# Kernel tuning notes

Hardware: AMD Instinct MI355X
Metric: run time of the kernel (lower is better)

## Reference

```python
import jax, jax.numpy as jnp
import numpy as np

B, S, T, D, H, DF = 2, 2048, 2048, 1024, 16, 4096
DK = D // H
EPS = 1e-5


def _linear_params(key, d_in, d_out):
    kw, kb = jax.random.split(key)
    s = 1.0 / np.sqrt(d_in)
    W = jax.random.uniform(kw, (d_out, d_in), jnp.float32, -s, s)
    b = jax.random.uniform(kb, (d_out,), jnp.float32, -s, s)
    return W, b


def setup_inputs() -> dict:
    key = jax.random.key(0)
    ks = jax.random.split(key, 16)
    inp = {}
    inp['x'] = jax.random.normal(ks[0], (B, S, D), jnp.float32)
    inp['enc_out'] = jax.random.normal(ks[1], (B, T, D), jnp.float32)
    inp['src_mask'] = jnp.ones((B, 1, 1, T), jnp.int32)
    inp['tgt_mask'] = jnp.tril(jnp.ones((S, S), jnp.int32))[None, None, :, :]
    # self-attn params
    for i, nm in enumerate(['q1', 'k1', 'v1', 'o1']):
        W, b = _linear_params(ks[2 + i], D, D)
        inp['W' + nm], inp['b' + nm] = W, b
    # cross-attn params
    for i, nm in enumerate(['q2', 'k2', 'v2', 'o2']):
        W, b = _linear_params(ks[6 + i], D, D)
        inp['W' + nm], inp['b' + nm] = W, b
    # FFN
    inp['Wf1'], inp['bf1'] = _linear_params(ks[10], D, DF)
    inp['Wf2'], inp['bf2'] = _linear_params(ks[11], DF, D)
    # LayerNorms
    for i in (1, 2, 3):
        inp[f'g{i}'] = jnp.ones((D,), jnp.float32)
        inp[f'be{i}'] = jnp.zeros((D,), jnp.float32)
    return inp


def _lin(x, W, b):
    return x @ W.T + b


def _ln(x, g, b):
    mu = jnp.mean(x, -1, keepdims=True)
    var = jnp.mean(jnp.square(x - mu), -1, keepdims=True)
    return (x - mu) * jax.lax.rsqrt(var + EPS) * g + b


def _mha(q_in, k_in, v_in, Wq, bq, Wk, bk, Wv, bv, Wo, bo, mask):
    Bq = q_in.shape[0]
    q = _lin(q_in, Wq, bq).reshape(Bq, -1, H, DK).transpose(0, 2, 1, 3)
    k = _lin(k_in, Wk, bk).reshape(Bq, -1, H, DK).transpose(0, 2, 1, 3)
    v = _lin(v_in, Wv, bv).reshape(Bq, -1, H, DK).transpose(0, 2, 1, 3)
    scores = jnp.einsum('bhqd,bhkd->bhqk', q, k) / np.sqrt(DK)
    scores = jnp.where(mask == 0, -jnp.inf, scores)
    attn = jax.nn.softmax(scores, axis=-1)
    out = jnp.einsum('bhqk,bhkd->bhqd', attn, v)
    out = out.transpose(0, 2, 1, 3).reshape(Bq, -1, H * DK)
    return _lin(out, Wo, bo)


def reference(x, enc_out, src_mask, tgt_mask,
              Wq1, bq1, Wk1, bk1, Wv1, bv1, Wo1, bo1,
              Wq2, bq2, Wk2, bk2, Wv2, bv2, Wo2, bo2,
              Wf1, bf1, Wf2, bf2,
              g1, be1, g2, be2, g3, be3):
    out = _mha(x, x, x, Wq1, bq1, Wk1, bk1, Wv1, bv1, Wo1, bo1, tgt_mask)
    x = _ln(x + out, g1, be1)
    out = _mha(x, enc_out, enc_out, Wq2, bq2, Wk2, bk2, Wv2, bv2, Wo2, bo2, src_mask)
    x = _ln(x + out, g2, be2)
    ff = _lin(jax.nn.relu(_lin(x, Wf1, bf1)), Wf2, bf2)
    return _ln(x + ff, g3, be3)
```

## Files before the change

kernel.cpp:

```cpp
#include <hip/hip_runtime.h>


typedef __bf16 bf16_t;
typedef bf16_t  bf16x8 __attribute__((ext_vector_type(8)));
typedef float   f32x4  __attribute__((ext_vector_type(4)));
typedef unsigned short ushort_t;
typedef ushort_t u16x8 __attribute__((ext_vector_type(8)));
typedef ushort_t u16x4 __attribute__((ext_vector_type(4)));

__device__ __forceinline__ float b2f(ushort_t u) {
    union { unsigned u; float f; } x; x.u = ((unsigned)u) << 16; return x.f;
}
__device__ __forceinline__ ushort_t f2b(float f) {
    union { float f; unsigned u; } x; x.f = f;
    unsigned r = x.u + 0x7fffu + ((x.u >> 16) & 1u);
    return (ushort_t)(r >> 16);
}
__device__ __forceinline__ unsigned pk2(float lo, float hi) {
    union { float f; unsigned u; } a, b; a.f = lo; b.f = hi;
    return (b.u & 0xffff0000u) | (a.u >> 16);
}

#define GLL(gp, lp)                                                            \
    __builtin_amdgcn_global_load_lds(                                          \
        (const __attribute__((address_space(1))) void*)(gp),                   \
        (__attribute__((address_space(3))) void*)(lp), 16, 0, 0)

__global__ __launch_bounds__(256) void conv_all(
    const float* __restrict__ x,   const float* __restrict__ enc,
    const float* __restrict__ w0, const float* __restrict__ w1,
    const float* __restrict__ w2, const float* __restrict__ w3,
    const float* __restrict__ w4, const float* __restrict__ w5,
    const float* __restrict__ w6, const float* __restrict__ w7,
    const float* __restrict__ wf1, const float* __restrict__ wf2,
    ushort_t* __restrict__ Xb, ushort_t* __restrict__ Eb,
    ushort_t* __restrict__ Wb)
{
    const int b = blockIdx.x;
    const float* src;
    ushort_t* dst;
    size_t blk;
    if (b < 2048)      { src = x;   dst = Xb; blk = b; }
    else if (b < 4096) { src = enc; dst = Eb; blk = b - 2048; }
    else if (b < 8192) {
        const int i = (b - 4096) >> 9;
        src = (i < 4) ? (i < 2 ? (i == 0 ? w0 : w1) : (i == 2 ? w2 : w3))
                      : (i < 6 ? (i == 4 ? w4 : w5) : (i == 6 ? w6 : w7));
        dst = Wb + (size_t)i * 1048576;
        blk = (b - 4096) & 511;
    }
    else if (b < 10240) { src = wf1; dst = Wb + (size_t)8  * 1048576; blk = b - 8192; }
    else                { src = wf2; dst = Wb + (size_t)12 * 1048576; blk = b - 10240; }

    const size_t e = blk * 2048 + (size_t)threadIdx.x * 8;
    const float4 a = *(const float4*)(src + e);
    const float4 c = *(const float4*)(src + e + 4);
    uint4 r;
    r.x = pk2(a.x, a.y); r.y = pk2(a.z, a.w);
    r.z = pk2(c.x, c.y); r.w = pk2(c.z, c.w);
    *(uint4*)(dst + e) = r;
}

template <int EPI, int TM, bool RF32, bool FUSED, bool SPLITA, bool SPLITC>
__global__ __launch_bounds__(256) void gemm_bt(
    const ushort_t* __restrict__ A, const ushort_t* __restrict__ A2,
    const ushort_t* __restrict__ W,
    const float* __restrict__ b1, const float* __restrict__ b2,
    const float* __restrict__ b3,
    const void* __restrict__ Rv,
    ushort_t* __restrict__ C, ushort_t* __restrict__ C2,
    int M, int N, int K)
{
    constexpr int IM = TM / 32;
    __shared__ __align__(16) ushort_t At[TM * 32];
    __shared__ __align__(16) ushort_t Bt[128 * 32];

    const int tid  = threadIdx.x;
    const int lane = tid & 63, w = tid >> 6;
    const int g = lane >> 4, qi = lane & 15;
    const int bm = blockIdx.y * TM, bn = blockIdx.x * 128;
    const int wm = (w >> 1) * (TM / 2), wn = (w & 1) * 64;

    const ushort_t* Ap = SPLITA ? ((bm < 2048) ? A : A2) : A;
    const int       am = SPLITA ? (bm & 2047) : bm;

    const int srow = lane >> 2;
    const int scol = (lane & 3) * 8;

    f32x4 acc[IM][4] = {};

    const int niter = K >> 5;
    for (int kt = 0; kt < niter; ++kt) {
        const int k0 = kt << 5;
        __syncthreads();
        if (TM == 128) {
#pragma unroll
            for (int c = 0; c < 2; ++c) {
                const int s = c * 4 + w;
                GLL(Ap + (size_t)(am + s * 16 + srow) * K + k0 + scol, At + s * 512);
            }
        } else {
            GLL(Ap + (size_t)(am + w * 16 + srow) * K + k0 + scol, At + w * 512);
        }
#pragma unroll
        for (int c = 0; c < 2; ++c) {
            const int s = c * 4 + w;
            GLL(W + (size_t)(bn + s * 16 + srow) * K + k0 + scol, Bt + s * 512);
        }
        __syncthreads();

        bf16x8 af[IM], bfr[4];
#pragma unroll
        for (int i = 0; i < IM; ++i)
            af[i] = *(const bf16x8*)(At + (wm + i * 16 + qi) * 32 + g * 8);
#pragma unroll
        for (int j = 0; j < 4; ++j)
            bfr[j] = *(const bf16x8*)(Bt + (wn + j * 16 + qi) * 32 + g * 8);
#pragma unroll
        for (int i = 0; i < IM; ++i)
#pragma unroll
            for (int j = 0; j < 4; ++j)
                acc[i][j] = __builtin_amdgcn_mfma_f32_16x16x32_bf16(
                    af[i], bfr[j], acc[i][j], 0, 0, 0);
    }

    const float* bp = FUSED ? (bn < 1024 ? b1 : (bn < 2048 ? b2 : b3)) : b1;
#pragma unroll
    for (int j = 0; j < 4; ++j) {
        const int n = bn + wn + j * 16 + qi;
        const int nl = n & 1023;
        const float bv = bp[nl];
#pragma unroll
        for (int i = 0; i < IM; ++i) {
#pragma unroll
            for (int r = 0; r < 4; ++r) {
                const int m = bm + wm + i * 16 + g * 4 + r;
                float v = acc[i][j][r] + bv;
                if (EPI == 2) {
                    v += RF32 ? ((const float*)Rv)[(size_t)m * N + n]
                              : b2f(((const ushort_t*)Rv)[(size_t)m * N + n]);
                }
                if (EPI == 3) v = v > 0.f ? v : 0.f;
                if (EPI == 1) {
                    const int which = FUSED ? (bn >> 10) : 0;
                    const int bb = m >> 11, s = m & 2047;
                    const int h = nl >> 6, dk = nl & 63;
                    const size_t dst = (size_t)which * 4194304 +
                        (((size_t)((bb << 4) + h)) * 2048 + s) * 64 + dk;
                    C[dst] = f2b(v);
                } else {
                    ushort_t* Cp = SPLITC ? (m < 2048 ? C : C2) : C;
                    const int mr = SPLITC ? (m & 2047) : m;
                    Cp[(size_t)mr * N + n] = f2b(v);
                }
            }
        }
    }
}

template <bool CAUSAL>
__global__ __launch_bounds__(256) void flash_attn(
    const ushort_t* __restrict__ Q, const ushort_t* __restrict__ K,
    const ushort_t* __restrict__ V, ushort_t* __restrict__ O, int S)
{
    __shared__ __align__(16) ushort_t Kt[2 * 32 * 32];
    __shared__ __align__(16) ushort_t Vt[64 * 40];
    __shared__ __align__(16) ushort_t Pl[4 * 16 * 32];

    const int tid = threadIdx.x, lane = tid & 63, w = tid >> 6;
    const int g = lane >> 4, qi = lane & 15;
    const int q2 = (qi >> 1) & 3;
    const int bh = blockIdx.y;
    const size_t base = (size_t)bh * S * 64;
    const int q0 = blockIdx.x * 64;
    const int qw = q0 + w * 16;

    const int krow2 = ((w & 1) << 4) + (lane >> 2);
    const int kcol2 = ((w >> 1) << 5) + ((lane & 3) << 3);

    bf16x8 qf0 = *(const bf16x8*)(Q + base + (size_t)(qw + qi) * 64 + g * 8);
    bf16x8 qf1 = *(const bf16x8*)(Q + base + (size_t)(qw + qi) * 64 + 32 + g * 8);

    f32x4 oacc[4] = {};
    float m_i = -1e30f, l_i = 0.f;

    const int ntiles = CAUSAL ? ((q0 >> 5) + 2) : (S >> 5);
    for (int t = 0; t < ntiles; ++t) {
        const int k0 = t << 5;
        u16x8 pk;
#pragma unroll
        for (int j = 0; j < 8; ++j)
            pk[j] = V[base + (size_t)(k0 + w * 8 + j) * 64 + lane];
        __syncthreads();
        GLL(K + base + (size_t)(k0 + krow2) * 64 + kcol2, Kt + w * 512);
        *(u16x8*)(Vt + lane * 40 + w * 8) = pk;
        __syncthreads();

        f32x4 st[2] = {};
        __builtin_amdgcn_s_setprio(1);
#pragma unroll
        for (int tt = 0; tt < 2; ++tt) {
            bf16x8 kf0 = *(const bf16x8*)(Kt + (tt * 16 + qi) * 32 + g * 8);
            bf16x8 kf1 = *(const bf16x8*)(Kt + 1024 + (tt * 16 + qi) * 32 + g * 8);
            st[tt] = __builtin_amdgcn_mfma_f32_16x16x32_bf16(kf0, qf0, st[tt], 0, 0, 0);
            st[tt] = __builtin_amdgcn_mfma_f32_16x16x32_bf16(kf1, qf1, st[tt], 0, 0, 0);
        }
        __builtin_amdgcn_s_setprio(0);

        if (CAUSAL && (k0 + 31 > qw)) {
#pragma unroll
            for (int tt = 0; tt < 2; ++tt)
#pragma unroll
                for (int r = 0; r < 4; ++r)
                    if (k0 + tt * 16 + g * 4 + r > qw + qi) st[tt][r] = -1e30f;
        }

        float mx = st[0][0];
#pragma unroll
        for (int r = 1; r < 4; ++r) mx = fmaxf(mx, st[0][r]);
#pragma unroll
        for (int r = 0; r < 4; ++r) mx = fmaxf(mx, st[1][r]);
        mx = fmaxf(mx, __shfl_xor(mx, 16));
        mx = fmaxf(mx, __shfl_xor(mx, 32));

        if (!__all(mx - m_i <= 64.f)) {
            const float m_new = fmaxf(m_i, mx);
            const float alpha = __expf((m_i - m_new) * 0.125f);
            float av[4];
#pragma unroll
            for (int r = 0; r < 4; ++r) av[r] = __shfl(alpha, g * 4 + r, 16);
#pragma unroll
            for (int dt = 0; dt < 4; ++dt)
#pragma unroll
                for (int r = 0; r < 4; ++r) oacc[dt][r] *= av[r];
            l_i *= alpha;
            m_i = m_new;
        }

        float p[2][4];
        float psum = 0.f;
#pragma unroll
        for (int tt = 0; tt < 2; ++tt)
#pragma unroll
            for (int r = 0; r < 4; ++r) {
                p[tt][r] = __expf((st[tt][r] - m_i) * 0.125f);
                psum += p[tt][r];
            }
        psum += __shfl_xor(psum, 16);
        psum += __shfl_xor(psum, 32);
        l_i += psum;

        ushort_t* pb = Pl + w * 512;
#pragma unroll
        for (int tt = 0; tt < 2; ++tt) {
            unsigned lo, hi;
            asm("v_cvt_pk_bf16_f32 %0, %1, %2" : "=v"(lo) : "v"(p[tt][0]), "v"(p[tt][1]));
            asm("v_cvt_pk_bf16_f32 %0, %1, %2" : "=v"(hi) : "v"(p[tt][2]), "v"(p[tt][3]));
            const int swc = (tt * 2 + (g >> 1)) ^ q2;
            uint2 pw; pw.x = lo; pw.y = hi;
            *(uint2*)(pb + qi * 32 + swc * 8 + (g & 1) * 4) = pw;
        }
        asm volatile("s_waitcnt lgkmcnt(0)" ::: "memory");
        __builtin_amdgcn_sched_barrier(0);
        bf16x8 pf = *(const bf16x8*)(pb + qi * 32 + ((g ^ q2) << 3));

        __builtin_amdgcn_s_setprio(1);
#pragma unroll
        for (int dt = 0; dt < 4; ++dt) {
            bf16x8 vf = *(const bf16x8*)(Vt + (dt * 16 + qi) * 40 + g * 8);
            oacc[dt] = __builtin_amdgcn_mfma_f32_16x16x32_bf16(pf, vf, oacc[dt], 0, 0, 0);
        }
        __builtin_amdgcn_s_setprio(0);
    }

    float lv[4];
#pragma unroll
    for (int r = 0; r < 4; ++r) lv[r] = 1.f / __shfl(l_i, g * 4 + r, 16);

    const int b = bh >> 4, h = bh & 15;
#pragma unroll
    for (int dt = 0; dt < 4; ++dt)
#pragma unroll
        for (int r = 0; r < 4; ++r) {
            const int row = b * S + qw + g * 4 + r;
            const int col = (h << 6) + dt * 16 + qi;
            O[(size_t)row * 1024 + col] = f2b(oacc[dt][r] * lv[r]);
        }
}

template <bool OUTF32>
__global__ __launch_bounds__(256) void ln_kernel(
    const ushort_t* __restrict__ X, const float* __restrict__ gam,
    const float* __restrict__ bet, void* __restrict__ Yv)
{
    const int row = blockIdx.x, tid = threadIdx.x;
    const int lane = tid & 63, w = tid >> 6;
    const size_t off = (size_t)row * 1024 + tid * 4;

    u16x4 xv = *(const u16x4*)(X + off);
    float f[4];
#pragma unroll
    for (int i = 0; i < 4; ++i) f[i] = b2f(xv[i]);

    float s = f[0] + f[1] + f[2] + f[3];
    float sq = f[0] * f[0] + f[1] * f[1] + f[2] * f[2] + f[3] * f[3];
#pragma unroll
    for (int o = 32; o; o >>= 1) {
        s  += __shfl_xor(s, o);
        sq += __shfl_xor(sq, o);
    }
    __shared__ float red[8];
    if (lane == 0) { red[w] = s; red[4 + w] = sq; }
    __syncthreads();
    s  = red[0] + red[1] + red[2] + red[3];
    sq = red[4] + red[5] + red[6] + red[7];

    const float mu = s * (1.f / 1024.f);
    const float var = sq * (1.f / 1024.f) - mu * mu;
    const float rs = rsqrtf(var + 1e-5f);

    const float4 gv = *(const float4*)(gam + tid * 4);
    const float4 bv = *(const float4*)(bet + tid * 4);
    float y0 = (f[0] - mu) * rs * gv.x + bv.x;
    float y1 = (f[1] - mu) * rs * gv.y + bv.y;
    float y2 = (f[2] - mu) * rs * gv.z + bv.z;
    float y3 = (f[3] - mu) * rs * gv.w + bv.w;

    if (OUTF32) {
        float4 yv; yv.x = y0; yv.y = y1; yv.z = y2; yv.w = y3;
        *(float4*)((float*)Yv + off) = yv;
    } else {
        u16x4 yv;
        yv[0] = f2b(y0); yv[1] = f2b(y1); yv[2] = f2b(y2); yv[3] = f2b(y3);
        *(u16x4*)((ushort_t*)Yv + off) = yv;
    }
}

extern "C" void kernel_launch(void* const* d_in, const int* in_sizes, int n_in,
                              void* d_out, int out_size, void* d_ws, size_t ws_size,
                              hipStream_t stream)
{
    const float* x   = (const float*)d_in[0];
    const float* enc = (const float*)d_in[1];
    const float* Wq1 = (const float*)d_in[4];
    const float* bq1 = (const float*)d_in[5];
    const float* Wk1 = (const float*)d_in[6];
    const float* bk1 = (const float*)d_in[7];
    const float* Wv1 = (const float*)d_in[8];
    const float* bv1 = (const float*)d_in[9];
    const float* Wo1 = (const float*)d_in[10];
    const float* bo1 = (const float*)d_in[11];
    const float* Wq2 = (const float*)d_in[12];
    const float* bq2 = (const float*)d_in[13];
    const float* Wk2 = (const float*)d_in[14];
    const float* bk2 = (const float*)d_in[15];
    const float* Wv2 = (const float*)d_in[16];
    const float* bv2 = (const float*)d_in[17];
    const float* Wo2 = (const float*)d_in[18];
    const float* bo2 = (const float*)d_in[19];
    const float* Wf1 = (const float*)d_in[20];
    const float* bf1 = (const float*)d_in[21];
    const float* Wf2 = (const float*)d_in[22];
    const float* bf2 = (const float*)d_in[23];
    const float* gm1 = (const float*)d_in[24];
    const float* be1 = (const float*)d_in[25];
    const float* gm2 = (const float*)d_in[26];
    const float* be2 = (const float*)d_in[27];
    const float* gm3 = (const float*)d_in[28];
    const float* be3 = (const float*)d_in[29];

    float*    out = (float*)d_out;
    ushort_t* ws  = (ushort_t*)d_ws;
    ushort_t* F2  = (ushort_t*)d_out;

    const size_t E = (size_t)4096 * 1024;
    ushort_t* P0 = ws;
    ushort_t* P1 = ws + 1 * E;
    ushort_t* P2 = ws + 2 * E;
    ushort_t* P3 = ws + 3 * E;
    ushort_t* P4 = ws + 4 * E;
    ushort_t* Wb = ws + 5 * E;

    const size_t M1 = 1048576;
    ushort_t* Wb_qkv1 = Wb;
    ushort_t* Wb_o1   = Wb + 3 * M1;
    ushort_t* Wb_q2   = Wb + 4 * M1;
    ushort_t* Wb_kv2  = Wb + 5 * M1;
    ushort_t* Wb_o2   = Wb + 7 * M1;
    ushort_t* Wb_f1   = Wb + 8 * M1;
    ushort_t* Wb_f2   = Wb + 12 * M1;

    const dim3 blk(256);
    const dim3 gA(32, 32);

    conv_all<<<12288, blk, 0, stream>>>(x, enc, Wq1, Wk1, Wv1, Wo1, Wq2, Wk2,
                                        Wv2, Wo2, Wf1, Wf2, P3, P4, Wb);

    gemm_bt<1, 128, false, true, false, false><<<dim3(24, 32), blk, 0, stream>>>(
        P3, nullptr, Wb_qkv1, bq1, bk1, bv1, nullptr, P0, nullptr, 4096, 3072, 1024);
    flash_attn<true><<<gA, blk, 0, stream>>>(P0, P1, P2, P3, 2048);
    gemm_bt<2, 64, true, false, false, false><<<dim3(8, 64), blk, 0, stream>>>(
        P3, nullptr, Wb_o1, bo1, bo1, bo1, x, P0, nullptr, 4096, 1024, 1024);
    ln_kernel<false><<<4096, blk, 0, stream>>>(P0, gm1, be1, P1);

    gemm_bt<1, 64, false, false, false, false><<<dim3(8, 64), blk, 0, stream>>>(
        P1, nullptr, Wb_q2, bq2, bq2, bq2, nullptr, P0, nullptr, 4096, 1024, 1024);
    gemm_bt<1, 128, false, true, false, false><<<dim3(16, 32), blk, 0, stream>>>(
        P4, nullptr, Wb_kv2, bk2, bv2, bv2, nullptr, P2, nullptr, 4096, 2048, 1024);
    flash_attn<false><<<gA, blk, 0, stream>>>(P0, P2, P3, P4, 2048);
    gemm_bt<2, 64, false, false, false, false><<<dim3(8, 64), blk, 0, stream>>>(
        P4, nullptr, Wb_o2, bo2, bo2, bo2, P1, P0, nullptr, 4096, 1024, 1024);
    ln_kernel<false><<<4096, blk, 0, stream>>>(P0, gm2, be2, P2);

    gemm_bt<3, 128, false, false, false, true><<<dim3(32, 32), blk, 0, stream>>>(
        P2, nullptr, Wb_f1, bf1, bf1, bf1, nullptr, P0, F2, 4096, 4096, 1024);
    gemm_bt<2, 64, false, false, true, false><<<dim3(8, 64), blk, 0, stream>>>(
        P0, F2, Wb_f2, bf2, bf2, bf2, P2, P3, nullptr, 4096, 1024, 4096);
    ln_kernel<true><<<4096, blk, 0, stream>>>(P3, gm3, be3, out);
}
```

Before: 647.2 us.

## Double-buffer K/V tiles in flash attention and defer row-sum reduction

The flash attention kernel now keeps two LDS buffers for the K and V tiles. It prefetches the next tile's K (via global_load_lds) and V (into registers) before computing on the current tile, and writes them after the PV MFMAs, so one barrier per iteration replaces two. The per-tile cross-lane shuffle reduction of the softmax denominator is moved out of the loop and done once at the end. This costs double the K/V LDS footprint and more live registers, which could lower occupancy.

```diff
diff --git a/kernel.cpp b/kernel.cpp
--- a/kernel.cpp
+++ b/kernel.cpp
@@ -163,8 +163,8 @@
     const ushort_t* __restrict__ Q, const ushort_t* __restrict__ K,
     const ushort_t* __restrict__ V, ushort_t* __restrict__ O, int S)
 {
-    __shared__ __align__(16) ushort_t Kt[2 * 32 * 32];
-    __shared__ __align__(16) ushort_t Vt[64 * 40];
+    __shared__ __align__(16) ushort_t Kt[2][2048];
+    __shared__ __align__(16) ushort_t Vt[2][64 * 40];
     __shared__ __align__(16) ushort_t Pl[4 * 16 * 32];
 
     const int tid = threadIdx.x, lane = tid & 63, w = tid >> 6;
@@ -180,28 +180,47 @@
 
     bf16x8 qf0 = *(const bf16x8*)(Q + base + (size_t)(qw + qi) * 64 + g * 8);
     bf16x8 qf1 = *(const bf16x8*)(Q + base + (size_t)(qw + qi) * 64 + 32 + g * 8);
+    asm volatile("" :: "v"(qf0), "v"(qf1));
 
     f32x4 oacc[4] = {};
-    float m_i = -1e30f, l_i = 0.f;
+    float m_i = -1e30f, lsum = 0.f;
 
     const int ntiles = CAUSAL ? ((q0 >> 5) + 2) : (S >> 5);
+
+    {
+        u16x8 vk0;
+#pragma unroll
+        for (int j = 0; j < 8; ++j)
+            vk0[j] = V[base + (size_t)(w * 8 + j) * 64 + lane];
+        GLL(K + base + (size_t)krow2 * 64 + kcol2, &Kt[0][w * 512]);
+        asm volatile("s_waitcnt vmcnt(0)" ::: "memory");
+        *(u16x8*)(&Vt[0][lane * 40 + w * 8]) = vk0;
+        asm volatile("s_waitcnt lgkmcnt(0)" ::: "memory");
+        __builtin_amdgcn_s_barrier();
+        __builtin_amdgcn_sched_barrier(0);
+    }
+
     for (int t = 0; t < ntiles; ++t) {
+        const int cur = t & 1;
         const int k0 = t << 5;
-        u16x8 pk;
-#pragma unroll
-        for (int j = 0; j < 8; ++j)
-            pk[j] = V[base + (size_t)(k0 + w * 8 + j) * 64 + lane];
-        __syncthreads();
-        GLL(K + base + (size_t)(k0 + krow2) * 64 + kcol2, Kt + w * 512);
-        *(u16x8*)(Vt + lane * 40 + w * 8) = pk;
-        __syncthreads();
+        const bool pre = (t + 1 < ntiles);
+
+        u16x8 vk2;
+        if (pre) {
+            const int kn = k0 + 32;
+#pragma unroll
+            for (int j = 0; j < 8; ++j)
+                vk2[j] = V[base + (size_t)(kn + w * 8 + j) * 64 + lane];
+            GLL(K + base + (size_t)(kn + krow2) * 64 + kcol2, &Kt[cur ^ 1][w * 512]);
+        }
+        __builtin_amdgcn_sched_barrier(0);
 
         f32x4 st[2] = {};
         __builtin_amdgcn_s_setprio(1);
 #pragma unroll
         for (int tt = 0; tt < 2; ++tt) {
-            bf16x8 kf0 = *(const bf16x8*)(Kt + (tt * 16 + qi) * 32 + g * 8);
-            bf16x8 kf1 = *(const bf16x8*)(Kt + 1024 + (tt * 16 + qi) * 32 + g * 8);
+            bf16x8 kf0 = *(const bf16x8*)(&Kt[cur][(tt * 16 + qi) * 32 + g * 8]);
+            bf16x8 kf1 = *(const bf16x8*)(&Kt[cur][1024 + (tt * 16 + qi) * 32 + g * 8]);
             st[tt] = __builtin_amdgcn_mfma_f32_16x16x32_bf16(kf0, qf0, st[tt], 0, 0, 0);
             st[tt] = __builtin_amdgcn_mfma_f32_16x16x32_bf16(kf1, qf1, st[tt], 0, 0, 0);
         }
@@ -233,22 +252,18 @@
             for (int dt = 0; dt < 4; ++dt)
 #pragma unroll
                 for (int r = 0; r < 4; ++r) oacc[dt][r] *= av[r];
-            l_i *= alpha;
+            lsum *= alpha;
             m_i = m_new;
         }
 
         float p[2][4];
-        float psum = 0.f;
 #pragma unroll
         for (int tt = 0; tt < 2; ++tt)
 #pragma unroll
             for (int r = 0; r < 4; ++r) {
                 p[tt][r] = __expf((st[tt][r] - m_i) * 0.125f);
-                psum += p[tt][r];
+                lsum += p[tt][r];
             }
-        psum += __shfl_xor(psum, 16);
-        psum += __shfl_xor(psum, 32);
-        l_i += psum;
 
         ushort_t* pb = Pl + w * 512;
 #pragma unroll
@@ -267,15 +282,26 @@
         __builtin_amdgcn_s_setprio(1);
 #pragma unroll
         for (int dt = 0; dt < 4; ++dt) {
-            bf16x8 vf = *(const bf16x8*)(Vt + (dt * 16 + qi) * 40 + g * 8);
+            bf16x8 vf = *(const bf16x8*)(&Vt[cur][(dt * 16 + qi) * 40 + g * 8]);
             oacc[dt] = __builtin_amdgcn_mfma_f32_16x16x32_bf16(pf, vf, oacc[dt], 0, 0, 0);
         }
         __builtin_amdgcn_s_setprio(0);
-    }
-
+
+        if (pre) {
+            asm volatile("s_waitcnt vmcnt(0)" ::: "memory");
+            __builtin_amdgcn_sched_barrier(0);
+            *(u16x8*)(&Vt[cur ^ 1][lane * 40 + w * 8]) = vk2;
+            asm volatile("s_waitcnt lgkmcnt(0)" ::: "memory");
+            __builtin_amdgcn_s_barrier();
+            __builtin_amdgcn_sched_barrier(0);
+        }
+    }
+
+    lsum += __shfl_xor(lsum, 16);
+    lsum += __shfl_xor(lsum, 32);
     float lv[4];
 #pragma unroll
-    for (int r = 0; r < 4; ++r) lv[r] = 1.f / __shfl(l_i, g * 4 + r, 16);
+    for (int r = 0; r < 4; ++r) lv[r] = 1.f / __shfl(lsum, g * 4 + r, 16);
 
     const int b = bh >> 4, h = bh & 15;
 #pragma unroll
```

Result: slower. 663.3 us (+2.5%).
